# Performance work log

Measured on AMD Instinct MI355X. Metric: run time of the kernel, lower is better.

Reference implementation:

```python
import jax, jax.numpy as jnp
import numpy as np

NFFT = 512
HOP = 256
N_FREQ = NFFT // 2


def _imdct_kernels():
    # Matches _get_imdct_kernels: windowed IMDCT cosine basis, shape [nfft, nfft//2]
    def kernel_fn(time, freq):
        win = np.sin(np.pi * (2 * time + 1) / (2.0 * NFFT))
        return np.cos(np.pi / NFFT * (2 * time + 1 + NFFT / 2.0) * (freq + 0.5)) * win
    k = np.fromfunction(kernel_fn, (NFFT, N_FREQ), dtype=np.float64)
    return jnp.asarray(k.astype(np.float32))  # [nfft, n_freq]


def setup_inputs() -> dict:
    key = jax.random.key(0)
    spec = jax.random.normal(key, (16, 1, N_FREQ, 4096), dtype=jnp.float32)
    return {"spec": spec, "kernels": _imdct_kernels()}


def reference(spec, kernels):
    # spec: [B, 1, n_freq, T]; kernels: [nfft, n_freq]
    B, _, _, T = spec.shape
    # conv2d with (n_freq,1) kernel == per-frame basis matmul over frequency
    frames = jnp.einsum('bft,kf->btk', spec[:, 0], kernels) * (4.0 / NFFT)  # [B, T, nfft]
    # conv_transpose2d with identity-diagonal kernel and stride=hop == overlap-add
    L = (T - 1) * HOP + NFFT
    idx = jnp.arange(T)[:, None] * HOP + jnp.arange(NFFT)[None, :]  # [T, nfft]
    out = jnp.zeros((B, L), dtype=spec.dtype).at[:, idx].add(frames)
    return out
```

## Files before the change

### kernel.cpp

```cpp
#include <hip/hip_runtime.h>
#include <stdint.h>

#define NFREQ 256
#define NB 16
#define NT 4096
#define LOUT 1048832
#define TROWS 65
#define TROW 132
#define BGRP 1088

typedef __bf16 bf16;
typedef __bf16 bf16x8 __attribute__((ext_vector_type(8)));
typedef float floatx4 __attribute__((ext_vector_type(4)));

__device__ inline uint32_t f_as_u(float x) { union { float f; uint32_t u; } v; v.f = x; return v.u; }
__device__ inline uint32_t bf16r(float x) {
    uint32_t u = f_as_u(x);
    return (u + 0x7fffu + ((u >> 16) & 1u)) >> 16;
}

__global__ __launch_bounds__(256) void build_kb(const float* __restrict__ ker,
                                                bf16* __restrict__ kb) {
    int idx = blockIdx.x * 256 + threadIdx.x;
    int r = idx >> 9, f = idx & 511;
    float v = (f < 256) ? ker[(r + 256) * 256 + f] : ker[r * 256 + (f - 256)];
    uint32_t rr = bf16r(v * 0.0078125f);
    union { uint16_t u; bf16 b; } o; o.u = (uint16_t)rr;
    kb[idx] = o.b;
}

__device__ inline void load_lds16(const bf16* g, void* l) {
    __builtin_amdgcn_global_load_lds((const __attribute__((address_space(1))) uint32_t*)g,
                                     (__attribute__((address_space(3))) uint32_t*)l,
                                     16, 0, 0);
}

__global__ __launch_bounds__(256, 2) void imdct_gemm(const float* __restrict__ spec,
                                                     const bf16* __restrict__ kb,
                                                     float* __restrict__ out) {
    __shared__ uint32_t Tt[TROWS * TROW];
    __shared__ uint8_t  Bs[32 * BGRP];

    const int jt = blockIdx.x;
    const int b  = blockIdx.y;
    const int tid = threadIdx.x, lane = tid & 63, w = tid >> 6;
    const int j0 = jt * 64;
    const float* sb = spec + (size_t)b * NFREQ * NT;

    {
        const int lpar = lane & 1, lt = lane >> 1;
        const int fpw = w * 32;
        for (int rb = 0; rb < 4; ++rb) {
            float v[16];
            #pragma unroll
            for (int i = 0; i < 16; ++i) {
                int r = rb * 16 + i;
                int tc = r >> 5, fpi = r & 31;
                int f = (fpw + fpi) * 2 + lpar;
                int t = j0 - 1 + tc * 32 + lt;
                v[i] = ((unsigned)t < (unsigned)NT) ? sb[(size_t)f * NT + t] : 0.0f;
            }
            #pragma unroll
            for (int i = 0; i < 16; i += 2) {
                int r = rb * 16 + i;
                int tc = r >> 5, fpi = r & 31;
                int tl = tc * 32 + lt;
                uint32_t h0 = bf16r(v[i]);     uint32_t o0 = (uint32_t)__shfl_xor((int)h0, 1);
                uint32_t h1 = bf16r(v[i + 1]); uint32_t o1 = (uint32_t)__shfl_xor((int)h1, 1);
                if (lpar == 0) {
                    uint2 pk; pk.x = (h0 & 0xffffu) | (o0 << 16); pk.y = (h1 & 0xffffu) | (o1 << 16);
                    *reinterpret_cast<uint2*>(&Tt[tl * TROW + fpw + fpi]) = pk;
                }
            }
        }
        int f = w * 64 + lane;
        int t = j0 + 63;
        float v = ((unsigned)t < (unsigned)NT) ? sb[(size_t)f * NT + t] : 0.0f;
        uint32_t h = bf16r(v); uint32_t o = (uint32_t)__shfl_xor((int)h, 1);
        if (lpar == 0) Tt[64 * TROW + w * 32 + lt] = (h & 0xffffu) | (o << 16);
    }

    const int row16 = lane & 15, q = lane >> 4;
    floatx4 acc[4][4] = {};
    const uint8_t* Tb = reinterpret_cast<const uint8_t*>(Tt);

    for (int kki = 0; kki < 8; ++kki) {
        #pragma unroll
        for (int g8 = 0; g8 < 8; ++g8) {
            int g = w * 8 + g8;
            const bf16* gsrc = kb + (size_t)(g * 8 + (lane >> 3)) * 512 + kki * 64 + (lane & 7) * 8;
            load_lds16(gsrc, Bs + g * BGRP);
        }
        __syncthreads();

        const int toff = (kki >= 4) ? 1 : 0;
        const int kbyte = (kki & 3) * 128;
        #pragma unroll
        for (int ks = 0; ks < 2; ++ks) {
            bf16x8 af[4], bfr[4];
            #pragma unroll
            for (int i = 0; i < 4; ++i)
                af[i] = *reinterpret_cast<const bf16x8*>(
                    Tb + (size_t)(i * 16 + row16 + toff) * 528 + kbyte + ks * 64 + q * 16);
            #pragma unroll
            for (int jn = 0; jn < 4; ++jn) {
                int n = w * 64 + jn * 16 + row16;
                bfr[jn] = *reinterpret_cast<const bf16x8*>(
                    Bs + (n >> 3) * BGRP + (n & 7) * 128 + ks * 64 + q * 16);
            }
            #pragma unroll
            for (int i = 0; i < 4; ++i)
                #pragma unroll
                for (int jn = 0; jn < 4; ++jn)
                    acc[i][jn] = __builtin_amdgcn_mfma_f32_16x16x32_bf16(af[i], bfr[jn], acc[i][jn], 0, 0, 0);
        }
        __syncthreads();
    }

    #pragma unroll
    for (int i = 0; i < 4; ++i) {
        #pragma unroll
        for (int e = 0; e < 4; ++e) {
            int j = j0 + i * 16 + q * 4 + e;
            if (j <= 4096) {
                float* orow = out + (size_t)b * LOUT + (size_t)j * 256 + w * 64;
                #pragma unroll
                for (int jn = 0; jn < 4; ++jn)
                    orow[jn * 16 + row16] = acc[i][jn][e];
            }
        }
    }
}

extern "C" void kernel_launch(void* const* d_in, const int* in_sizes, int n_in,
                              void* d_out, int out_size, void* d_ws, size_t ws_size,
                              hipStream_t stream) {
    const float* spec = (const float*)d_in[0];
    const float* ker  = (const float*)d_in[1];
    float* out = (float*)d_out;

    bf16* kb = (bf16*)d_ws;

    build_kb<<<512, 256, 0, stream>>>(ker, kb);
    imdct_gemm<<<dim3(65, NB), 256, 0, stream>>>(spec, kb, out);
}
```

Before: 145.6 us.

## Load basis fragments directly from global memory instead of staging through LDS

The basis matrix is pre-permuted into a fragment-friendly layout (k-chunks of 32 by n) so each wave can read its MFMA B operands straight from global/L2 with 16-byte loads. This drops the per-iteration LDS staging buffer and its two barriers, and raises the occupancy hint from 2 to 4 blocks per CU now that LDS use is smaller. The trade-off is more global/L2 traffic for the basis operand, with latency that now has to be hidden by occupancy instead of explicit staging. A barrier is added after the spectrum tile is written to LDS.

```diff
diff --git a/kernel.cpp b/kernel.cpp
--- a/kernel.cpp
+++ b/kernel.cpp
@@ -7,7 +7,6 @@
 #define LOUT 1048832
 #define TROWS 65
 #define TROW 132
-#define BGRP 1088
 
 typedef __bf16 bf16;
 typedef __bf16 bf16x8 __attribute__((ext_vector_type(8)));
@@ -20,26 +19,19 @@
 }
 
 __global__ __launch_bounds__(256) void build_kb(const float* __restrict__ ker,
-                                                bf16* __restrict__ kb) {
+                                                bf16* __restrict__ kbF) {
     int idx = blockIdx.x * 256 + threadIdx.x;
-    int r = idx >> 9, f = idx & 511;
-    float v = (f < 256) ? ker[(r + 256) * 256 + f] : ker[r * 256 + (f - 256)];
+    int n = idx >> 9, f = idx & 511;
+    float v = (f < 256) ? ker[(n + 256) * 256 + f] : ker[n * 256 + (f - 256)];
     uint32_t rr = bf16r(v * 0.0078125f);
     union { uint16_t u; bf16 b; } o; o.u = (uint16_t)rr;
-    kb[idx] = o.b;
+    kbF[((size_t)(f >> 5) * 256 + n) * 32 + (f & 31)] = o.b;
 }
 
-__device__ inline void load_lds16(const bf16* g, void* l) {
-    __builtin_amdgcn_global_load_lds((const __attribute__((address_space(1))) uint32_t*)g,
-                                     (__attribute__((address_space(3))) uint32_t*)l,
-                                     16, 0, 0);
-}
-
-__global__ __launch_bounds__(256, 2) void imdct_gemm(const float* __restrict__ spec,
-                                                     const bf16* __restrict__ kb,
+__global__ __launch_bounds__(256, 4) void imdct_gemm(const float* __restrict__ spec,
+                                                     const bf16* __restrict__ kbF,
                                                      float* __restrict__ out) {
     __shared__ uint32_t Tt[TROWS * TROW];
-    __shared__ uint8_t  Bs[32 * BGRP];
 
     const int jt = blockIdx.x;
     const int b  = blockIdx.y;
@@ -79,42 +71,34 @@
         uint32_t h = bf16r(v); uint32_t o = (uint32_t)__shfl_xor((int)h, 1);
         if (lpar == 0) Tt[64 * TROW + w * 32 + lt] = (h & 0xffffu) | (o << 16);
     }
+    __syncthreads();
 
     const int row16 = lane & 15, q = lane >> 4;
     floatx4 acc[4][4] = {};
     const uint8_t* Tb = reinterpret_cast<const uint8_t*>(Tt);
+    const bf16* kbw = kbF + (size_t)w * 64 * 32;
 
     for (int kki = 0; kki < 8; ++kki) {
-        #pragma unroll
-        for (int g8 = 0; g8 < 8; ++g8) {
-            int g = w * 8 + g8;
-            const bf16* gsrc = kb + (size_t)(g * 8 + (lane >> 3)) * 512 + kki * 64 + (lane & 7) * 8;
-            load_lds16(gsrc, Bs + g * BGRP);
-        }
-        __syncthreads();
-
         const int toff = (kki >= 4) ? 1 : 0;
         const int kbyte = (kki & 3) * 128;
         #pragma unroll
         for (int ks = 0; ks < 2; ++ks) {
+            const int kchunk = kki * 2 + ks;
             bf16x8 af[4], bfr[4];
             #pragma unroll
             for (int i = 0; i < 4; ++i)
                 af[i] = *reinterpret_cast<const bf16x8*>(
                     Tb + (size_t)(i * 16 + row16 + toff) * 528 + kbyte + ks * 64 + q * 16);
             #pragma unroll
-            for (int jn = 0; jn < 4; ++jn) {
-                int n = w * 64 + jn * 16 + row16;
+            for (int jn = 0; jn < 4; ++jn)
                 bfr[jn] = *reinterpret_cast<const bf16x8*>(
-                    Bs + (n >> 3) * BGRP + (n & 7) * 128 + ks * 64 + q * 16);
-            }
+                    kbw + (size_t)kchunk * 8192 + (jn * 16 + row16) * 32 + q * 8);
             #pragma unroll
             for (int i = 0; i < 4; ++i)
                 #pragma unroll
                 for (int jn = 0; jn < 4; ++jn)
                     acc[i][jn] = __builtin_amdgcn_mfma_f32_16x16x32_bf16(af[i], bfr[jn], acc[i][jn], 0, 0, 0);
         }
-        __syncthreads();
     }
 
     #pragma unroll
@@ -139,8 +123,8 @@
     const float* ker  = (const float*)d_in[1];
     float* out = (float*)d_out;
 
-    bf16* kb = (bf16*)d_ws;
+    bf16* kbF = (bf16*)d_ws;
 
-    build_kb<<<512, 256, 0, stream>>>(ker, kb);
-    imdct_gemm<<<dim3(65, NB), 256, 0, stream>>>(spec, kb, out);
+    build_kb<<<512, 256, 0, stream>>>(ker, kbF);
+    imdct_gemm<<<dim3(65, NB), 256, 0, stream>>>(spec, kbF, out);
 }
```

New measurement: 142.8 us. Within noise of the previous version (-1.9%).
